# Kernel tuning notes

Measured on AMD Instinct MI355X. Metric: run time of the kernel, lower is better.

Reference implementation:

```python
import jax, jax.numpy as jnp
import numpy as np

N_NODES = 100000
N_EDGES = 1600000
D_IN = 64
D_OUT = 64


def setup_inputs() -> dict:
    key = jax.random.key(0)
    k1, k2, k3, k4 = jax.random.split(key, 4)
    x = jax.random.normal(k1, (N_NODES, D_IN), dtype=jnp.float32)
    edge_index = jax.random.randint(k2, (2, N_EDGES), 0, N_NODES, dtype=jnp.int64)
    # MLP params (torch Linear stores [out,in]; here stored [in,out] for x @ W)
    s1 = (6.0 / (D_IN + D_OUT)) ** 0.5  # xavier_uniform bound
    s2 = (6.0 / (D_OUT + D_OUT)) ** 0.5
    W1 = jax.random.uniform(k3, (D_IN, D_OUT), dtype=jnp.float32, minval=-s1, maxval=s1)
    b1 = jnp.zeros((D_OUT,), dtype=jnp.float32)
    W2 = jax.random.uniform(k4, (D_OUT, D_OUT), dtype=jnp.float32, minval=-s2, maxval=s2)
    b2 = jnp.zeros((D_OUT,), dtype=jnp.float32)
    return {"x": x, "edge_index": edge_index, "W1": W1, "b1": b1, "W2": W2, "b2": b2}


def reference(x, edge_index, W1, b1, W2, b2):
    # Eval mode: F.dropout is identity when training=False.
    src, dst = edge_index[0], edge_index[1]
    # GIN aggregation: sum of neighbor features scattered to destination nodes
    agg = jax.ops.segment_sum(x[src], dst, num_segments=N_NODES)  # [N, D_IN]
    h = x + agg  # (1 + eps) * x + agg, eps = 0 (GINConv default)
    h = jax.nn.relu(h @ W1 + b1)
    return h @ W2 + b2
```

## Files before the change

### kernel.cpp

```cpp
#include <hip/hip_runtime.h>

#define N_NODES 100000
#define N_EDGES 1600000

#define SPAN 256
#define NB 391
#define NBLK_A 256
#define EPB (N_EDGES / NBLK_A)

#define SCAN_CHUNK 2048
#define SCAN_BLOCKS ((N_NODES + SCAN_CHUNK - 1) / SCAN_CHUNK)

typedef __attribute__((ext_vector_type(8))) short bf16x8;
typedef __attribute__((ext_vector_type(4))) float f32x4;

static __device__ __forceinline__ unsigned short f2bf(float f) {
    unsigned u = __float_as_uint(f);
    unsigned r = (u + 0x7FFF + ((u >> 16) & 1)) >> 16;
    return (unsigned short)r;
}


__global__ __launch_bounds__(512) void count_buckets(const int* __restrict__ ei,
                                                     int* __restrict__ M) {
    __shared__ int hist[NB];
    int tid = threadIdx.x;
    for (int i = tid; i < NB; i += 512) hist[i] = 0;
    __syncthreads();
    int e0 = blockIdx.x * EPB;
    for (int e = e0 + tid; e < e0 + EPB; e += 512)
        atomicAdd(&hist[ei[N_EDGES + e] >> 8], 1);
    __syncthreads();
    for (int i = tid; i < NB; i += 512) M[blockIdx.x * NB + i] = hist[i];
}

__global__ void col_scan(int* __restrict__ M, int* __restrict__ bcount) {
    int b = blockIdx.x * blockDim.x + threadIdx.x;
    if (b >= NB) return;
    int s = 0;
    for (int k = 0; k < NBLK_A; ++k) {
        int idx = k * NB + b;
        int t = M[idx];
        M[idx] = s;
        s += t;
    }
    bcount[b] = s;
}

__global__ __launch_bounds__(512) void bucket_base(const int* __restrict__ bcount,
                                                   int* __restrict__ bbase) {
    __shared__ int s[512];
    int tid = threadIdx.x;
    int v = (tid < NB) ? bcount[tid] : 0;
    s[tid] = v;
    __syncthreads();
    for (int off = 1; off < 512; off <<= 1) {
        int t = (tid >= off) ? s[tid - off] : 0;
        __syncthreads();
        s[tid] += t;
        __syncthreads();
    }
    if (tid < NB) bbase[tid] = s[tid] - v;
    if (tid == NB - 1) bbase[NB] = s[tid];
}

__global__ __launch_bounds__(512) void bin_edges(const int* __restrict__ ei,
                                                 const int* __restrict__ M,
                                                 const int* __restrict__ bbase,
                                                 int* __restrict__ binned) {
    __shared__ int sbase[NB];
    __shared__ int cur[NB];
    int tid = threadIdx.x;
    for (int i = tid; i < NB; i += 512) {
        sbase[i] = bbase[i] + M[blockIdx.x * NB + i];
        cur[i] = 0;
    }
    __syncthreads();
    int e0 = blockIdx.x * EPB;
    for (int e = e0 + tid; e < e0 + EPB; e += 512) {
        int d = ei[N_EDGES + e];
        int s = ei[e];
        int b = d >> 8;
        int r = atomicAdd(&cur[b], 1);
        binned[sbase[b] + r] = (s << 8) | (d & 255);
    }
}

__global__ __launch_bounds__(512) void bucket_sort(const int* __restrict__ binned,
                                                   const int* __restrict__ bbase,
                                                   int* __restrict__ csr,
                                                   int* __restrict__ offs) {
    __shared__ int lh[256];
    __shared__ int ls[256];
    __shared__ int lc[256];
    int tid = threadIdx.x;
    int b = blockIdx.x;
    int base = bbase[b];
    int cnt = bbase[b + 1] - base;

    if (tid < 256) lh[tid] = 0;
    __syncthreads();
    for (int i = tid; i < cnt; i += 512)
        atomicAdd(&lh[binned[base + i] & 255], 1);
    __syncthreads();

    int own = 0;
    if (tid < 256) {
        own = lh[tid];
        ls[tid] = own;
    }
    __syncthreads();
    for (int off = 1; off < 256; off <<= 1) {
        int t = (tid < 256 && tid >= off) ? ls[tid - off] : 0;
        __syncthreads();
        if (tid < 256) ls[tid] += t;
        __syncthreads();
    }

    if (tid < 256) {
        int node = b * SPAN + tid;
        if (node < N_NODES) offs[node] = base + ls[tid];
    }

    int ex = (tid < 256) ? (ls[tid] - own) : 0;
    __syncthreads();
    if (tid < 256) {
        ls[tid] = ex;
        lc[tid] = 0;
    }
    __syncthreads();
    for (int i = tid; i < cnt; i += 512) {
        int en = binned[base + i];
        int ld = en & 255;
        int r = atomicAdd(&lc[ld], 1);
        csr[base + ls[ld] + r] = en >> 8;
    }
}

__global__ __launch_bounds__(512) void gather_mfma(
    const float4* __restrict__ x4, const int* __restrict__ offs,
    const int* __restrict__ csr, float* __restrict__ out,
    const float* __restrict__ W1, const float* __restrict__ b1,
    const float* __restrict__ W2, const float* __restrict__ b2) {

    __shared__ unsigned short shA[16][72];
    __shared__ unsigned short sh1[16][72];
    __shared__ unsigned short W1t[64][72];
    __shared__ unsigned short W2t[64][72];

    int tid = threadIdx.x;
    int w = tid >> 6;
    int lane = tid & 63;

    {
        int j = lane;
        int kc = w;
        unsigned p1[4], p2[4];
#pragma unroll
        for (int h = 0; h < 4; ++h) {
            float a0 = W1[(kc * 8 + 2 * h) * 64 + j];
            float a1 = W1[(kc * 8 + 2 * h + 1) * 64 + j];
            p1[h] = (unsigned)f2bf(a0) | ((unsigned)f2bf(a1) << 16);
            float c0 = W2[(kc * 8 + 2 * h) * 64 + j];
            float c1 = W2[(kc * 8 + 2 * h + 1) * 64 + j];
            p2[h] = (unsigned)f2bf(c0) | ((unsigned)f2bf(c1) << 16);
        }
        *(uint4*)&W1t[j][kc * 8] = make_uint4(p1[0], p1[1], p1[2], p1[3]);
        *(uint4*)&W2t[j][kc * 8] = make_uint4(p2[0], p2[1], p2[2], p2[3]);
    }

    int s = lane >> 4;
    int c = lane & 15;
    int nA = blockIdx.x * 16 + 2 * w;
    int nB = nA + 1;
    int stA = (nA == 0) ? 0 : offs[nA - 1];
    int enA = offs[nA];
    int stB = offs[nB - 1];
    int enB = offs[nB];

    float4 accA = make_float4(0.f, 0.f, 0.f, 0.f);
    float4 accB = accA;
    if (s == 0) {
        accA = x4[(size_t)nA * 16 + c];
        accB = x4[(size_t)nB * 16 + c];
    }

    for (int bA = stA, bB = stB; bA < enA || bB < enB; bA += 16, bB += 16) {
        int pA = bA + s, pB = bB + s;
        int a0 = (pA      < enA) ? csr[pA]      : -1;
        int a1 = (pA + 4  < enA) ? csr[pA + 4]  : -1;
        int a2 = (pA + 8  < enA) ? csr[pA + 8]  : -1;
        int a3 = (pA + 12 < enA) ? csr[pA + 12] : -1;
        int b0 = (pB      < enB) ? csr[pB]      : -1;
        int b1i = (pB + 4 < enB) ? csr[pB + 4]  : -1;
        int b2i = (pB + 8 < enB) ? csr[pB + 8]  : -1;
        int b3i = (pB + 12 < enB) ? csr[pB + 12] : -1;
        float4 vA0 = x4[(size_t)max(a0, 0) * 16 + c];
        float4 vA1 = x4[(size_t)max(a1, 0) * 16 + c];
        float4 vA2 = x4[(size_t)max(a2, 0) * 16 + c];
        float4 vA3 = x4[(size_t)max(a3, 0) * 16 + c];
        float4 vB0 = x4[(size_t)max(b0, 0) * 16 + c];
        float4 vB1 = x4[(size_t)max(b1i, 0) * 16 + c];
        float4 vB2 = x4[(size_t)max(b2i, 0) * 16 + c];
        float4 vB3 = x4[(size_t)max(b3i, 0) * 16 + c];
        if (a0 >= 0) { accA.x += vA0.x; accA.y += vA0.y; accA.z += vA0.z; accA.w += vA0.w; }
        if (a1 >= 0) { accA.x += vA1.x; accA.y += vA1.y; accA.z += vA1.z; accA.w += vA1.w; }
        if (a2 >= 0) { accA.x += vA2.x; accA.y += vA2.y; accA.z += vA2.z; accA.w += vA2.w; }
        if (a3 >= 0) { accA.x += vA3.x; accA.y += vA3.y; accA.z += vA3.z; accA.w += vA3.w; }
        if (b0 >= 0) { accB.x += vB0.x; accB.y += vB0.y; accB.z += vB0.z; accB.w += vB0.w; }
        if (b1i >= 0) { accB.x += vB1.x; accB.y += vB1.y; accB.z += vB1.z; accB.w += vB1.w; }
        if (b2i >= 0) { accB.x += vB2.x; accB.y += vB2.y; accB.z += vB2.z; accB.w += vB2.w; }
        if (b3i >= 0) { accB.x += vB3.x; accB.y += vB3.y; accB.z += vB3.z; accB.w += vB3.w; }
    }

    accA.x += __shfl_xor(accA.x, 16); accA.y += __shfl_xor(accA.y, 16);
    accA.z += __shfl_xor(accA.z, 16); accA.w += __shfl_xor(accA.w, 16);
    accA.x += __shfl_xor(accA.x, 32); accA.y += __shfl_xor(accA.y, 32);
    accA.z += __shfl_xor(accA.z, 32); accA.w += __shfl_xor(accA.w, 32);
    accB.x += __shfl_xor(accB.x, 16); accB.y += __shfl_xor(accB.y, 16);
    accB.z += __shfl_xor(accB.z, 16); accB.w += __shfl_xor(accB.w, 16);
    accB.x += __shfl_xor(accB.x, 32); accB.y += __shfl_xor(accB.y, 32);
    accB.z += __shfl_xor(accB.z, 32); accB.w += __shfl_xor(accB.w, 32);

    if (s == 0) {
        ushort4 ra, rb;
        ra.x = f2bf(accA.x); ra.y = f2bf(accA.y);
        ra.z = f2bf(accA.z); ra.w = f2bf(accA.w);
        rb.x = f2bf(accB.x); rb.y = f2bf(accB.y);
        rb.z = f2bf(accB.z); rb.w = f2bf(accB.w);
        *(ushort4*)&shA[2 * w][c * 4] = ra;
        *(ushort4*)&shA[2 * w + 1][c * 4] = rb;
    }
    __syncthreads();

    int row = lane & 15;
    int kg = lane >> 4;

    bf16x8 w20, w21;
    if (w >= 4) {
        int jj = (w - 4) * 16 + row;
        w20 = *(bf16x8*)&W2t[jj][kg * 8];
        w21 = *(bf16x8*)&W2t[jj][32 + kg * 8];
    }

    if (w < 4) {
        int jj = w * 16 + row;
        bf16x8 a0 = *(bf16x8*)&shA[row][kg * 8];
        bf16x8 a1 = *(bf16x8*)&shA[row][32 + kg * 8];
        bf16x8 w0 = *(bf16x8*)&W1t[jj][kg * 8];
        bf16x8 w1 = *(bf16x8*)&W1t[jj][32 + kg * 8];
        f32x4 d = {0.f, 0.f, 0.f, 0.f};
        d = __builtin_amdgcn_mfma_f32_16x16x32_bf16(a0, w0, d, 0, 0, 0);
        d = __builtin_amdgcn_mfma_f32_16x16x32_bf16(a1, w1, d, 0, 0, 0);
        float bias = b1[jj];
#pragma unroll
        for (int i = 0; i < 4; ++i) {
            float v = fmaxf(d[i] + bias, 0.f);
            sh1[kg * 4 + i][jj] = f2bf(v);
        }
    }
    __syncthreads();

    if (w >= 4) {
        int jj = (w - 4) * 16 + row;
        bf16x8 a0 = *(bf16x8*)&sh1[row][kg * 8];
        bf16x8 a1 = *(bf16x8*)&sh1[row][32 + kg * 8];
        f32x4 d = {0.f, 0.f, 0.f, 0.f};
        d = __builtin_amdgcn_mfma_f32_16x16x32_bf16(a0, w20, d, 0, 0, 0);
        d = __builtin_amdgcn_mfma_f32_16x16x32_bf16(a1, w21, d, 0, 0, 0);
        float bias = b2[jj];
        int nbase = blockIdx.x * 16 + kg * 4;
#pragma unroll
        for (int i = 0; i < 4; ++i)
            out[(size_t)(nbase + i) * 64 + jj] = d[i] + bias;
    }
}

__global__ __launch_bounds__(512) void gather_mlp(
    const float4* __restrict__ x4, const int* __restrict__ offs,
    const int* __restrict__ csr, float* __restrict__ out,
    const float* __restrict__ W1, const float* __restrict__ b1,
    const float* __restrict__ W2, const float* __restrict__ b2) {
    __shared__ float sW1[64][64];
    __shared__ float sW2[64][64];
    __shared__ float sb1[64];
    __shared__ float sb2[64];
    __shared__ float sh[8][64];
    __shared__ float sh1[8][64];

    int tid = threadIdx.x;
    for (int i = tid; i < 4096; i += 512) {
        sW1[i >> 6][i & 63] = W1[i];
        sW2[i >> 6][i & 63] = W2[i];
    }
    if (tid < 64) {
        sb1[tid] = b1[tid];
        sb2[tid] = b2[tid];
    }

    int local = tid >> 6;
    int lane = tid & 63;
    int s = lane >> 4;
    int c = lane & 15;
    int node = blockIdx.x * 8 + local;

    int start = (node == 0) ? 0 : offs[node - 1];
    int end = offs[node];

    float4 acc = make_float4(0.f, 0.f, 0.f, 0.f);
    float4 self = x4[(size_t)node * 16 + c];
    if (s == 0) acc = self;

    for (int b = start; b < end; b += 16) {
        int p = b + s;
        int i0 = (p < end) ? csr[p] : -1;
        int i1 = (p + 4 < end) ? csr[p + 4] : -1;
        int i2 = (p + 8 < end) ? csr[p + 8] : -1;
        int i3 = (p + 12 < end) ? csr[p + 12] : -1;
        float4 v0 = x4[(size_t)max(i0, 0) * 16 + c];
        float4 v1 = x4[(size_t)max(i1, 0) * 16 + c];
        float4 v2 = x4[(size_t)max(i2, 0) * 16 + c];
        float4 v3 = x4[(size_t)max(i3, 0) * 16 + c];
        if (i0 >= 0) { acc.x += v0.x; acc.y += v0.y; acc.z += v0.z; acc.w += v0.w; }
        if (i1 >= 0) { acc.x += v1.x; acc.y += v1.y; acc.z += v1.z; acc.w += v1.w; }
        if (i2 >= 0) { acc.x += v2.x; acc.y += v2.y; acc.z += v2.z; acc.w += v2.w; }
        if (i3 >= 0) { acc.x += v3.x; acc.y += v3.y; acc.z += v3.z; acc.w += v3.w; }
    }

    acc.x += __shfl_xor(acc.x, 16); acc.y += __shfl_xor(acc.y, 16);
    acc.z += __shfl_xor(acc.z, 16); acc.w += __shfl_xor(acc.w, 16);
    acc.x += __shfl_xor(acc.x, 32); acc.y += __shfl_xor(acc.y, 32);
    acc.z += __shfl_xor(acc.z, 32); acc.w += __shfl_xor(acc.w, 32);

    __syncthreads();
    if (s == 0) *(float4*)&sh[local][c * 4] = acc;
    __syncthreads();

    int j = lane;
    float a1 = sb1[j];
#pragma unroll
    for (int k = 0; k < 64; ++k) a1 = fmaf(sh[local][k], sW1[k][j], a1);
    a1 = fmaxf(a1, 0.0f);
    sh1[local][j] = a1;
    __syncthreads();

    float a2 = sb2[j];
#pragma unroll
    for (int k = 0; k < 64; ++k) a2 = fmaf(sh1[local][k], sW2[k][j], a2);
    out[(size_t)node * 64 + j] = a2;
}

__global__ void zero_ints(int* __restrict__ p, int n) {
    int i = blockIdx.x * blockDim.x + threadIdx.x;
    if (i < n) p[i] = 0;
}

__global__ void count_deg(const int* __restrict__ ei, int* __restrict__ deg) {
    int e = blockIdx.x * blockDim.x + threadIdx.x;
    if (e < N_EDGES) atomicAdd(&deg[ei[N_EDGES + e]], 1);
}

__global__ __launch_bounds__(256) void scan_a(const int* __restrict__ deg,
                                              int* __restrict__ offs,
                                              int* __restrict__ bsum) {
    __shared__ int lds[256];
    int tid = threadIdx.x;
    int base = blockIdx.x * SCAN_CHUNK + tid * 8;
    int v[8], ex[8];
    int run = 0;
#pragma unroll
    for (int k = 0; k < 8; ++k) {
        v[k] = (base + k < N_NODES) ? deg[base + k] : 0;
        ex[k] = run;
        run += v[k];
    }
    lds[tid] = run;
    __syncthreads();
    for (int off = 1; off < 256; off <<= 1) {
        int t = (tid >= off) ? lds[tid - off] : 0;
        __syncthreads();
        lds[tid] += t;
        __syncthreads();
    }
    int prefix = lds[tid] - run;
#pragma unroll
    for (int k = 0; k < 8; ++k)
        if (base + k < N_NODES) offs[base + k] = prefix + ex[k];
    if (tid == 0) bsum[blockIdx.x] = lds[255];
}

__global__ void scan_c(int* __restrict__ offs, const int* __restrict__ bsum) {
    int i = blockIdx.x * blockDim.x + threadIdx.x;
    if (i >= N_NODES) return;
    int chunk = i / SCAN_CHUNK;
    int add = 0;
    for (int t = 0; t < chunk; ++t) add += bsum[t];
    offs[i] += add;
}

__global__ void fill_csr(const int* __restrict__ ei, int* __restrict__ offs,
                         int* __restrict__ csr) {
    int e = blockIdx.x * blockDim.x + threadIdx.x;
    if (e >= N_EDGES) return;
    int src = ei[e];
    int dst = ei[N_EDGES + e];
    int pos = atomicAdd(&offs[dst], 1);
    csr[pos] = src;
}

__global__ void init_h(const float4* __restrict__ x, float4* __restrict__ h,
                       int n4) {
    int i = blockIdx.x * blockDim.x + threadIdx.x;
    if (i < n4) h[i] = x[i];
}

__global__ void scatter_add(const float4* __restrict__ x4,
                            const int* __restrict__ ei,
                            float* __restrict__ h) {
    long long i = (long long)blockIdx.x * blockDim.x + threadIdx.x;
    if (i >= (long long)N_EDGES * 16) return;
    int e = (int)(i >> 4);
    int lane = (int)(i & 15);
    int src = ei[e];
    int dst = ei[N_EDGES + e];
    float4 v = x4[(long long)src * 16 + lane];
    float* p = h + (long long)dst * 64 + lane * 4;
    unsafeAtomicAdd(p + 0, v.x);
    unsafeAtomicAdd(p + 1, v.y);
    unsafeAtomicAdd(p + 2, v.z);
    unsafeAtomicAdd(p + 3, v.w);
}

__global__ __launch_bounds__(256) void mlp(float* __restrict__ h,
                                           const float* __restrict__ W1,
                                           const float* __restrict__ b1,
                                           const float* __restrict__ W2,
                                           const float* __restrict__ b2) {
    __shared__ float sW1[64][64];
    __shared__ float sW2[64][64];
    __shared__ float sb1[64];
    __shared__ float sb2[64];
    __shared__ float sh[4][64];
    __shared__ float sh1[4][64];
    int tid = threadIdx.x;
    for (int i = tid; i < 4096; i += 256) {
        sW1[i >> 6][i & 63] = W1[i];
        sW2[i >> 6][i & 63] = W2[i];
    }
    if (tid < 64) { sb1[tid] = b1[tid]; sb2[tid] = b2[tid]; }
    __syncthreads();
    int local = tid >> 6, j = tid & 63;
    int node = blockIdx.x * 4 + local;
    sh[local][j] = h[(long long)node * 64 + j];
    __syncthreads();
    float acc = sb1[j];
#pragma unroll
    for (int k = 0; k < 64; ++k) acc = fmaf(sh[local][k], sW1[k][j], acc);
    acc = fmaxf(acc, 0.0f);
    sh1[local][j] = acc;
    __syncthreads();
    float acc2 = sb2[j];
#pragma unroll
    for (int k = 0; k < 64; ++k) acc2 = fmaf(sh1[local][k], sW2[k][j], acc2);
    h[(long long)node * 64 + j] = acc2;
}

extern "C" void kernel_launch(void* const* d_in, const int* in_sizes, int n_in,
                              void* d_out, int out_size, void* d_ws, size_t ws_size,
                              hipStream_t stream) {
    const float* x = (const float*)d_in[0];
    const int* ei = (const int*)d_in[1];
    const float* W1 = (const float*)d_in[2];
    const float* b1 = (const float*)d_in[3];
    const float* W2 = (const float*)d_in[4];
    const float* b2 = (const float*)d_in[5];
    float* out = (float*)d_out;

    size_t need_csr = (size_t)(N_NODES + NBLK_A * NB + NB + (NB + 1) +
                               2 * N_EDGES) * sizeof(int);
    size_t need_mid = (size_t)(2 * N_NODES + SCAN_BLOCKS + N_EDGES) * sizeof(int);

    if (ws_size >= need_csr) {
        int* offs = (int*)d_ws;
        int* M = offs + N_NODES;
        int* bcount = M + NBLK_A * NB;
        int* bbase = bcount + NB;
        int* binned = bbase + (NB + 1);
        int* csr = binned + N_EDGES;

        count_buckets<<<NBLK_A, 512, 0, stream>>>(ei, M);
        col_scan<<<(NB + 255) / 256, 256, 0, stream>>>(M, bcount);
        bucket_base<<<1, 512, 0, stream>>>(bcount, bbase);
        bin_edges<<<NBLK_A, 512, 0, stream>>>(ei, M, bbase, binned);
        bucket_sort<<<NB, 512, 0, stream>>>(binned, bbase, csr, offs);
        gather_mfma<<<N_NODES / 16, 512, 0, stream>>>((const float4*)x, offs,
                                                      csr, out, W1, b1, W2, b2);
    } else if (ws_size >= need_mid) {
        int* deg = (int*)d_ws;
        int* offs = deg + N_NODES;
        int* bsum = offs + N_NODES;
        int* csr = bsum + SCAN_BLOCKS;

        zero_ints<<<(N_NODES + 255) / 256, 256, 0, stream>>>(deg, N_NODES);
        count_deg<<<(N_EDGES + 255) / 256, 256, 0, stream>>>(ei, deg);
        scan_a<<<SCAN_BLOCKS, 256, 0, stream>>>(deg, offs, bsum);
        scan_c<<<(N_NODES + 255) / 256, 256, 0, stream>>>(offs, bsum);
        fill_csr<<<(N_EDGES + 255) / 256, 256, 0, stream>>>(ei, offs, csr);
        gather_mlp<<<N_NODES / 8, 512, 0, stream>>>((const float4*)x, offs,
                                                    csr, out, W1, b1, W2, b2);
    } else {
        int n4 = N_NODES * 64 / 4;
        init_h<<<(n4 + 255) / 256, 256, 0, stream>>>((const float4*)x,
                                                     (float4*)out, n4);
        long long nwork = (long long)N_EDGES * 16;
        scatter_add<<<(int)((nwork + 255) / 256), 256, 0, stream>>>(
            (const float4*)x, ei, out);
        mlp<<<N_NODES / 4, 256, 0, stream>>>(out, W1, b1, W2, b2);
    }
}
```

Before: 112.2 us.

## Parallelize column scan, fold bucket-base scan into consumers, fast-path full gather chunks

The serial per-column scan, which had one thread per bucket looping over 256 blocks, becomes one block per bucket running a shared-memory parallel scan. The separate single-block bucket_base kernel is removed, and the 391-entry prefix sum is instead recomputed redundantly inside bin_edges and bucket_sort, which drops one launch. In the gather loop, a branch-free fast path handles 16-edge chunks that are fully in range for both nodes, skipping the per-element bounds checks and masked adds. The cost is extra redundant scan work in every block of two kernels, plus more code in the gather loop.

```diff
diff --git a/kernel.cpp b/kernel.cpp
--- a/kernel.cpp
+++ b/kernel.cpp
@@ -34,48 +34,48 @@
     for (int i = tid; i < NB; i += 512) M[blockIdx.x * NB + i] = hist[i];
 }
 
-__global__ void col_scan(int* __restrict__ M, int* __restrict__ bcount) {
-    int b = blockIdx.x * blockDim.x + threadIdx.x;
-    if (b >= NB) return;
-    int s = 0;
-    for (int k = 0; k < NBLK_A; ++k) {
-        int idx = k * NB + b;
-        int t = M[idx];
-        M[idx] = s;
-        s += t;
-    }
-    bcount[b] = s;
-}
-
-__global__ __launch_bounds__(512) void bucket_base(const int* __restrict__ bcount,
-                                                   int* __restrict__ bbase) {
-    __shared__ int s[512];
-    int tid = threadIdx.x;
-    int v = (tid < NB) ? bcount[tid] : 0;
-    s[tid] = v;
-    __syncthreads();
-    for (int off = 1; off < 512; off <<= 1) {
-        int t = (tid >= off) ? s[tid - off] : 0;
-        __syncthreads();
-        s[tid] += t;
-        __syncthreads();
-    }
-    if (tid < NB) bbase[tid] = s[tid] - v;
-    if (tid == NB - 1) bbase[NB] = s[tid];
+__global__ __launch_bounds__(256) void col_scan(int* __restrict__ M,
+                                                int* __restrict__ bcount) {
+    __shared__ int s[256];
+    int b = blockIdx.x;
+    int t = threadIdx.x;
+    int v = M[t * NB + b];
+    s[t] = v;
+    __syncthreads();
+    for (int off = 1; off < 256; off <<= 1) {
+        int u = (t >= off) ? s[t - off] : 0;
+        __syncthreads();
+        s[t] += u;
+        __syncthreads();
+    }
+    M[t * NB + b] = s[t] - v;
+    if (t == 255) bcount[b] = s[255];
 }
 
 __global__ __launch_bounds__(512) void bin_edges(const int* __restrict__ ei,
                                                  const int* __restrict__ M,
-                                                 const int* __restrict__ bbase,
+                                                 const int* __restrict__ bcount,
                                                  int* __restrict__ binned) {
+    __shared__ int sb[512];
     __shared__ int sbase[NB];
     __shared__ int cur[NB];
     int tid = threadIdx.x;
-    for (int i = tid; i < NB; i += 512) {
-        sbase[i] = bbase[i] + M[blockIdx.x * NB + i];
-        cur[i] = 0;
-    }
-    __syncthreads();
+
+    int v = (tid < NB) ? bcount[tid] : 0;
+    sb[tid] = v;
+    __syncthreads();
+    for (int off = 1; off < 512; off <<= 1) {
+        int t = (tid >= off) ? sb[tid - off] : 0;
+        __syncthreads();
+        sb[tid] += t;
+        __syncthreads();
+    }
+    if (tid < NB) {
+        sbase[tid] = (sb[tid] - v) + M[blockIdx.x * NB + tid];
+        cur[tid] = 0;
+    }
+    __syncthreads();
+
     int e0 = blockIdx.x * EPB;
     for (int e = e0 + tid; e < e0 + EPB; e += 512) {
         int d = ei[N_EDGES + e];
@@ -87,16 +87,30 @@
 }
 
 __global__ __launch_bounds__(512) void bucket_sort(const int* __restrict__ binned,
-                                                   const int* __restrict__ bbase,
+                                                   const int* __restrict__ bcount,
                                                    int* __restrict__ csr,
                                                    int* __restrict__ offs) {
+    __shared__ int sb[512];
     __shared__ int lh[256];
     __shared__ int ls[256];
     __shared__ int lc[256];
+    __shared__ int base_sh;
     int tid = threadIdx.x;
     int b = blockIdx.x;
-    int base = bbase[b];
-    int cnt = bbase[b + 1] - base;
+
+    int v = (tid < NB) ? bcount[tid] : 0;
+    sb[tid] = v;
+    __syncthreads();
+    for (int off = 1; off < 512; off <<= 1) {
+        int t = (tid >= off) ? sb[tid - off] : 0;
+        __syncthreads();
+        sb[tid] += t;
+        __syncthreads();
+    }
+    if (tid == b) base_sh = sb[tid] - v;
+    __syncthreads();
+    int base = base_sh;
+    int cnt = bcount[b];
 
     if (tid < 256) lh[tid] = 0;
     __syncthreads();
@@ -187,30 +201,51 @@
 
     for (int bA = stA, bB = stB; bA < enA || bB < enB; bA += 16, bB += 16) {
         int pA = bA + s, pB = bB + s;
-        int a0 = (pA      < enA) ? csr[pA]      : -1;
-        int a1 = (pA + 4  < enA) ? csr[pA + 4]  : -1;
-        int a2 = (pA + 8  < enA) ? csr[pA + 8]  : -1;
-        int a3 = (pA + 12 < enA) ? csr[pA + 12] : -1;
-        int b0 = (pB      < enB) ? csr[pB]      : -1;
-        int b1i = (pB + 4 < enB) ? csr[pB + 4]  : -1;
-        int b2i = (pB + 8 < enB) ? csr[pB + 8]  : -1;
-        int b3i = (pB + 12 < enB) ? csr[pB + 12] : -1;
-        float4 vA0 = x4[(size_t)max(a0, 0) * 16 + c];
-        float4 vA1 = x4[(size_t)max(a1, 0) * 16 + c];
-        float4 vA2 = x4[(size_t)max(a2, 0) * 16 + c];
-        float4 vA3 = x4[(size_t)max(a3, 0) * 16 + c];
-        float4 vB0 = x4[(size_t)max(b0, 0) * 16 + c];
-        float4 vB1 = x4[(size_t)max(b1i, 0) * 16 + c];
-        float4 vB2 = x4[(size_t)max(b2i, 0) * 16 + c];
-        float4 vB3 = x4[(size_t)max(b3i, 0) * 16 + c];
-        if (a0 >= 0) { accA.x += vA0.x; accA.y += vA0.y; accA.z += vA0.z; accA.w += vA0.w; }
-        if (a1 >= 0) { accA.x += vA1.x; accA.y += vA1.y; accA.z += vA1.z; accA.w += vA1.w; }
-        if (a2 >= 0) { accA.x += vA2.x; accA.y += vA2.y; accA.z += vA2.z; accA.w += vA2.w; }
-        if (a3 >= 0) { accA.x += vA3.x; accA.y += vA3.y; accA.z += vA3.z; accA.w += vA3.w; }
-        if (b0 >= 0) { accB.x += vB0.x; accB.y += vB0.y; accB.z += vB0.z; accB.w += vB0.w; }
-        if (b1i >= 0) { accB.x += vB1.x; accB.y += vB1.y; accB.z += vB1.z; accB.w += vB1.w; }
-        if (b2i >= 0) { accB.x += vB2.x; accB.y += vB2.y; accB.z += vB2.z; accB.w += vB2.w; }
-        if (b3i >= 0) { accB.x += vB3.x; accB.y += vB3.y; accB.z += vB3.z; accB.w += vB3.w; }
+        if (bA + 16 <= enA && bB + 16 <= enB) {
+            int a0 = csr[pA], a1 = csr[pA + 4], a2 = csr[pA + 8], a3 = csr[pA + 12];
+            int b0 = csr[pB], b1i = csr[pB + 4], b2i = csr[pB + 8], b3i = csr[pB + 12];
+            float4 vA0 = x4[(size_t)a0 * 16 + c];
+            float4 vA1 = x4[(size_t)a1 * 16 + c];
+            float4 vA2 = x4[(size_t)a2 * 16 + c];
+            float4 vA3 = x4[(size_t)a3 * 16 + c];
+            float4 vB0 = x4[(size_t)b0 * 16 + c];
+            float4 vB1 = x4[(size_t)b1i * 16 + c];
+            float4 vB2 = x4[(size_t)b2i * 16 + c];
+            float4 vB3 = x4[(size_t)b3i * 16 + c];
+            accA.x += vA0.x + vA1.x + vA2.x + vA3.x;
+            accA.y += vA0.y + vA1.y + vA2.y + vA3.y;
+            accA.z += vA0.z + vA1.z + vA2.z + vA3.z;
+            accA.w += vA0.w + vA1.w + vA2.w + vA3.w;
+            accB.x += vB0.x + vB1.x + vB2.x + vB3.x;
+            accB.y += vB0.y + vB1.y + vB2.y + vB3.y;
+            accB.z += vB0.z + vB1.z + vB2.z + vB3.z;
+            accB.w += vB0.w + vB1.w + vB2.w + vB3.w;
+        } else {
+            int a0 = (pA      < enA) ? csr[pA]      : -1;
+            int a1 = (pA + 4  < enA) ? csr[pA + 4]  : -1;
+            int a2 = (pA + 8  < enA) ? csr[pA + 8]  : -1;
+            int a3 = (pA + 12 < enA) ? csr[pA + 12] : -1;
+            int b0 = (pB      < enB) ? csr[pB]      : -1;
+            int b1i = (pB + 4 < enB) ? csr[pB + 4]  : -1;
+            int b2i = (pB + 8 < enB) ? csr[pB + 8]  : -1;
+            int b3i = (pB + 12 < enB) ? csr[pB + 12] : -1;
+            float4 vA0 = x4[(size_t)max(a0, 0) * 16 + c];
+            float4 vA1 = x4[(size_t)max(a1, 0) * 16 + c];
+            float4 vA2 = x4[(size_t)max(a2, 0) * 16 + c];
+            float4 vA3 = x4[(size_t)max(a3, 0) * 16 + c];
+            float4 vB0 = x4[(size_t)max(b0, 0) * 16 + c];
+            float4 vB1 = x4[(size_t)max(b1i, 0) * 16 + c];
+            float4 vB2 = x4[(size_t)max(b2i, 0) * 16 + c];
+            float4 vB3 = x4[(size_t)max(b3i, 0) * 16 + c];
+            if (a0 >= 0) { accA.x += vA0.x; accA.y += vA0.y; accA.z += vA0.z; accA.w += vA0.w; }
+            if (a1 >= 0) { accA.x += vA1.x; accA.y += vA1.y; accA.z += vA1.z; accA.w += vA1.w; }
+            if (a2 >= 0) { accA.x += vA2.x; accA.y += vA2.y; accA.z += vA2.z; accA.w += vA2.w; }
+            if (a3 >= 0) { accA.x += vA3.x; accA.y += vA3.y; accA.z += vA3.z; accA.w += vA3.w; }
+            if (b0 >= 0) { accB.x += vB0.x; accB.y += vB0.y; accB.z += vB0.z; accB.w += vB0.w; }
+            if (b1i >= 0) { accB.x += vB1.x; accB.y += vB1.y; accB.z += vB1.z; accB.w += vB1.w; }
+            if (b2i >= 0) { accB.x += vB2.x; accB.y += vB2.y; accB.z += vB2.z; accB.w += vB2.w; }
+            if (b3i >= 0) { accB.x += vB3.x; accB.y += vB3.y; accB.z += vB3.z; accB.w += vB3.w; }
+        }
     }
 
     accA.x += __shfl_xor(accA.x, 16); accA.y += __shfl_xor(accA.y, 16);
@@ -476,7 +511,7 @@
     const float* b2 = (const float*)d_in[5];
     float* out = (float*)d_out;
 
-    size_t need_csr = (size_t)(N_NODES + NBLK_A * NB + NB + (NB + 1) +
+    size_t need_csr = (size_t)(N_NODES + NBLK_A * NB + NB +
                                2 * N_EDGES) * sizeof(int);
     size_t need_mid = (size_t)(2 * N_NODES + SCAN_BLOCKS + N_EDGES) * sizeof(int);
 
@@ -484,15 +519,13 @@
         int* offs = (int*)d_ws;
         int* M = offs + N_NODES;
         int* bcount = M + NBLK_A * NB;
-        int* bbase = bcount + NB;
-        int* binned = bbase + (NB + 1);
+        int* binned = bcount + NB;
         int* csr = binned + N_EDGES;
 
         count_buckets<<<NBLK_A, 512, 0, stream>>>(ei, M);
-        col_scan<<<(NB + 255) / 256, 256, 0, stream>>>(M, bcount);
-        bucket_base<<<1, 512, 0, stream>>>(bcount, bbase);
-        bin_edges<<<NBLK_A, 512, 0, stream>>>(ei, M, bbase, binned);
-        bucket_sort<<<NB, 512, 0, stream>>>(binned, bbase, csr, offs);
+        col_scan<<<NB, 256, 0, stream>>>(M, bcount);
+        bin_edges<<<NBLK_A, 512, 0, stream>>>(ei, M, bcount, binned);
+        bucket_sort<<<NB, 512, 0, stream>>>(binned, bcount, csr, offs);
         gather_mfma<<<N_NODES / 16, 512, 0, stream>>>((const float4*)x, offs,
                                                       csr, out, W1, b1, W2, b2);
     } else if (ws_size >= need_mid) {
```

Result: faster. 102.5 us (-8.6%).
